# Performance work log

Measured on AMD Instinct MI355X. Metric: run time of the kernel, lower is better.

The kernel has to match this reference:

```python
import jax, jax.numpy as jnp
import numpy as np

N_HEADS = 16
HEAD_DIM = 128
EPS = 1e-6


def _rmsnorm(t, w):
    # RMSNorm over last dim (head_dim)
    var = jnp.mean(jnp.square(t), axis=-1, keepdims=True)
    return t * jax.lax.rsqrt(var + EPS) * w


def _apply_rope(t, freqs):
    # t: [b, s, h, d]; freqs: [s, 1, d//2, 2, 2]
    b, s, h, d = t.shape
    t2 = t.reshape(b, s, h, 2, d // 2)
    t_ = jnp.moveaxis(t2, -2, -1)[..., None, :].astype(jnp.float32)  # [b,s,h,d/2,1,2]
    out = freqs[..., 0] * t_[..., 0] + freqs[..., 1] * t_[..., 1]    # [b,s,h,d/2,2]
    out = jnp.moveaxis(out, -1, -2).reshape(b, s, h, d)
    return out.astype(t.dtype)


def setup_inputs() -> dict:
    key = jax.random.key(0)
    ks = jax.random.split(key, 8)
    B, S, D = 2, 2048, 2048
    inner = N_HEADS * HEAD_DIM
    sc = 1.0 / np.sqrt(D)
    return {
        "x": jax.random.normal(ks[0], (B, S, D), jnp.float32),
        "rope_emb": jax.random.normal(ks[1], (S, 1, HEAD_DIM // 2, 2, 2), jnp.float32),
        "Wq": jax.random.normal(ks[2], (inner, D), jnp.float32) * sc,
        "Wk": jax.random.normal(ks[3], (inner, D), jnp.float32) * sc,
        "Wv": jax.random.normal(ks[4], (inner, D), jnp.float32) * sc,
        "Wo": jax.random.normal(ks[5], (D, inner), jnp.float32) * sc,
        "q_norm_w": jnp.ones((HEAD_DIM,), jnp.float32),
        "k_norm_w": jnp.ones((HEAD_DIM,), jnp.float32),
    }


def reference(x, rope_emb, Wq, Wk, Wv, Wo, q_norm_w, k_norm_w):
    b, s, _ = x.shape
    h, d = N_HEADS, HEAD_DIM
    q = (x @ Wq.T).reshape(b, s, h, d)
    k = (x @ Wk.T).reshape(b, s, h, d)
    v = (x @ Wv.T).reshape(b, s, h, d)
    q = _apply_rope(_rmsnorm(q, q_norm_w), rope_emb)
    k = _apply_rope(_rmsnorm(k, k_norm_w), rope_emb)
    # SDPA, heads-first layout
    qh = jnp.transpose(q, (0, 2, 1, 3))  # [b,h,s,d]
    kh = jnp.transpose(k, (0, 2, 1, 3))
    vh = jnp.transpose(v, (0, 2, 1, 3))
    scale = 1.0 / np.sqrt(d)
    scores = jnp.einsum('bhqd,bhkd->bhqk', qh, kh) * scale
    attn = jax.nn.softmax(scores, axis=-1)
    out = jnp.einsum('bhqk,bhkd->bhqd', attn, vh)  # [b,h,s,d]
    out = jnp.transpose(out, (0, 2, 1, 3)).reshape(b, s, h * d)
    return out @ Wo.T
```

## Files before the change

kernel.cpp:

```cpp
#include <hip/hip_runtime.h>
#include <hip/hip_bf16.h>
#include <stdint.h>

typedef __bf16 bf16;
typedef __bf16 bf16x4 __attribute__((ext_vector_type(4)));
typedef __bf16 bf16x8 __attribute__((ext_vector_type(8)));
typedef float f32x4 __attribute__((ext_vector_type(4)));
typedef float f32x16 __attribute__((ext_vector_type(16)));

#define N_HEADS 16
#define HEAD_DIM 128
#define SEQ 2048
#define DIM 2048
#define BATCH 2
#define MROWS (BATCH * SEQ)
#define NQKV (3 * DIM)
#define SM_SCALE 0.08838834764831845f
#define QSCALE_L2E 0.12751743343563824f
#define SMAX_L2E 34.624680981335122f

#define MFMA16(a, b, c) __builtin_amdgcn_mfma_f32_16x16x32_bf16(a, b, c, 0, 0, 0)

__device__ __forceinline__ bf16 f2b(float f) {
  union { __hip_bfloat16 h; bf16 b; } u;
  u.h = __float2bfloat16(f);
  return u.b;
}

__device__ __forceinline__ uint32_t pack2(float a, float b) {
  union { __hip_bfloat16 h; unsigned short s; } ua, ub;
  ua.h = __float2bfloat16(a); ub.h = __float2bfloat16(b);
  return (uint32_t)ua.s | ((uint32_t)ub.s << 16);
}

__device__ __forceinline__ void async16(const bf16* g, bf16* l) {
  __builtin_amdgcn_global_load_lds(
      (__attribute__((address_space(1))) void*)(uintptr_t)g,
      (__attribute__((address_space(3))) void*)(uintptr_t)l,
      16, 0, 0);
}

__global__ __launch_bounds__(256) void cvt_kernel(const float* __restrict__ src,
                                                  bf16* __restrict__ dst, int n) {
  int i = (blockIdx.x * 256 + threadIdx.x) * 8;
  if (i >= n) return;
  float4 a = *(const float4*)(src + i);
  float4 b = *(const float4*)(src + i + 4);
  bf16x8 o;
  o[0] = f2b(a.x); o[1] = f2b(a.y); o[2] = f2b(a.z); o[3] = f2b(a.w);
  o[4] = f2b(b.x); o[5] = f2b(b.y); o[6] = f2b(b.z); o[7] = f2b(b.w);
  *(bf16x8*)(dst + i) = o;
}

__global__ __launch_bounds__(256) void cvt_w4(const float* __restrict__ w0,
                                              const float* __restrict__ w1,
                                              const float* __restrict__ w2,
                                              const float* __restrict__ w3,
                                              bf16* __restrict__ wqkv,
                                              bf16* __restrict__ wo) {
  const int per = (DIM * DIM) / 8 / 256;
  int which = blockIdx.x / per;
  int i = (blockIdx.x % per) * 256 * 8 + threadIdx.x * 8;
  const float* src = which == 0 ? w0 : which == 1 ? w1 : which == 2 ? w2 : w3;
  bf16* dst = which < 3 ? wqkv + (size_t)which * DIM * DIM : wo;
  float4 a = *(const float4*)(src + i);
  float4 b = *(const float4*)(src + i + 4);
  bf16x8 o;
  o[0] = f2b(a.x); o[1] = f2b(a.y); o[2] = f2b(a.z); o[3] = f2b(a.w);
  o[4] = f2b(b.x); o[5] = f2b(b.y); o[6] = f2b(b.z); o[7] = f2b(b.w);
  *(bf16x8*)(dst + i) = o;
}


#define GBAR() asm volatile("s_barrier" ::: "memory")
#define GWAITL() do { asm volatile("s_waitcnt lgkmcnt(0)" ::: "memory"); \
                      __builtin_amdgcn_sched_barrier(0); } while (0)

__device__ __forceinline__ void g256_stage_half(const bf16* gbase, bf16* lbase,
                                                int w, int lane, int t, int hf) {
  const int kt = t * 64;
#pragma unroll
  for (int i = 0; i < 2; i++) {
    const int rbase = hf * 128 + w * 16 + i * 8;
    const int r = rbase + (lane >> 3);
    async16(gbase + (size_t)r * 2048 + kt + 8 * ((lane & 7) ^ (r & 7)),
            lbase + rbase * 64);
  }
}

__device__ __forceinline__ void g256_lda(const bf16* lbase, int wm, int lm,
                                         int quad, int mh, bf16x8 a[4][2]) {
#pragma unroll
  for (int f = 0; f < 4; f++) {
    const int row = wm * 128 + mh * 64 + f * 16 + lm;
    const char* p = (const char*)lbase + row * 128;
    const int sw = (row & 7) << 4;
#pragma unroll
    for (int s = 0; s < 2; s++)
      a[f][s] = *(const bf16x8*)(p + ((s * 64 + quad * 16) ^ sw));
  }
}

__device__ __forceinline__ void g256_ldb(const bf16* lbase, int wn, int lm,
                                         int quad, int nh, bf16x8 bb[2][2]) {
#pragma unroll
  for (int g = 0; g < 2; g++) {
    const int row = wn * 64 + nh * 32 + g * 16 + lm;
    const char* p = (const char*)lbase + row * 128;
    const int sw = (row & 7) << 4;
#pragma unroll
    for (int s = 0; s < 2; s++)
      bb[g][s] = *(const bf16x8*)(p + ((s * 64 + quad * 16) ^ sw));
  }
}

__device__ __forceinline__ void g256_mma(f32x4 acc[8][4], bf16x8 a[4][2],
                                         bf16x8 bb[2][2], int mh, int nh) {
  __builtin_amdgcn_s_setprio(1);
#pragma unroll
  for (int s = 0; s < 2; s++)
#pragma unroll
    for (int f = 0; f < 4; f++)
#pragma unroll
      for (int g = 0; g < 2; g++)
        acc[mh * 4 + f][nh * 2 + g] =
            MFMA16(a[f][s], bb[g][s], acc[mh * 4 + f][nh * 2 + g]);
  __builtin_amdgcn_s_setprio(0);
}

__device__ __forceinline__ void gemm256_mainloop(
    const bf16* __restrict__ Ag, const bf16* __restrict__ Bg,
    bf16* sA0, bf16* sA1, bf16* sB0, bf16* sB1, f32x4 acc[8][4],
    int w, int lane, int wm, int wn, int lm, int quad) {
  g256_stage_half(Ag, sA0, w, lane, 0, 0);
  g256_stage_half(Ag, sA0, w, lane, 0, 1);
  g256_stage_half(Bg, sB0, w, lane, 0, 0);
  g256_stage_half(Bg, sB0, w, lane, 0, 1);
  g256_stage_half(Ag, sA1, w, lane, 1, 0);
  g256_stage_half(Ag, sA1, w, lane, 1, 1);
  asm volatile("s_waitcnt vmcnt(0)" ::: "memory");
  GBAR();

  bf16x8 a0[4][2], a1[4][2], bb[2][2];

  for (int i = 0; i < 16; i++) {
    const int t1 = 2 * i + 1;
    const int t2 = t1 + 1 < 32 ? t1 + 1 : 31;
    const int t3 = t1 + 2 < 32 ? t1 + 2 : 31;
    g256_lda(sA0, wm, lm, quad, 0, a0);
    g256_ldb(sB0, wn, lm, quad, 0, bb);
    g256_stage_half(Bg, sB1, w, lane, t1, 0);
    GBAR(); GWAITL();
    g256_mma(acc, a0, bb, 0, 0);
    GBAR();
    g256_lda(sA0, wm, lm, quad, 1, a1);
    g256_stage_half(Bg, sB1, w, lane, t1, 1);
    GBAR(); GWAITL();
    g256_mma(acc, a1, bb, 1, 0);
    GBAR();
    g256_ldb(sB0, wn, lm, quad, 1, bb);
    g256_stage_half(Ag, sA0, w, lane, t2, 0);
    GBAR(); GWAITL();
    g256_mma(acc, a1, bb, 1, 1);
    GBAR();
    g256_stage_half(Ag, sA0, w, lane, t2, 1);
    asm volatile("s_waitcnt vmcnt(4)" ::: "memory");
    GBAR(); GWAITL();
    g256_mma(acc, a0, bb, 0, 1);
    GBAR();
    g256_lda(sA1, wm, lm, quad, 0, a0);
    g256_ldb(sB1, wn, lm, quad, 0, bb);
    g256_stage_half(Bg, sB0, w, lane, t2, 0);
    GBAR(); GWAITL();
    g256_mma(acc, a0, bb, 0, 0);
    GBAR();
    g256_lda(sA1, wm, lm, quad, 1, a1);
    g256_stage_half(Bg, sB0, w, lane, t2, 1);
    GBAR(); GWAITL();
    g256_mma(acc, a1, bb, 1, 0);
    GBAR();
    g256_ldb(sB1, wn, lm, quad, 1, bb);
    g256_stage_half(Ag, sA1, w, lane, t3, 0);
    GBAR(); GWAITL();
    g256_mma(acc, a1, bb, 1, 1);
    GBAR();
    g256_stage_half(Ag, sA1, w, lane, t3, 1);
    asm volatile("s_waitcnt vmcnt(4)" ::: "memory");
    GBAR(); GWAITL();
    g256_mma(acc, a0, bb, 0, 1);
    GBAR();
  }
  asm volatile("s_waitcnt vmcnt(0)" ::: "memory");
}

__global__ __launch_bounds__(512, 2) void gemm_qkv(const bf16* __restrict__ X,
                                                   const bf16* __restrict__ W,
                                                   bf16* __restrict__ Q,
                                                   bf16* __restrict__ Kv,
                                                   bf16* __restrict__ VT) {
  __shared__ __align__(16) bf16 sA[2][256 * 64];
  __shared__ __align__(16) bf16 sB[2][256 * 64];
  const int t = threadIdx.x, w = t >> 6, lane = t & 63;
  const int lm = lane & 15, quad = lane >> 4;
  const int wm = w >> 2, wn = w & 3;
  const int bid = blockIdx.x;
  const int swz = (bid & 7) * 48 + (bid >> 3);
  const int bm = swz / 24, bn = swz % 24;
  const int rowBase = bm * 256, colBase = bn * 256;

  f32x4 acc[8][4];
  f32x4 z = {0.f, 0.f, 0.f, 0.f};
#pragma unroll
  for (int i = 0; i < 8; i++)
#pragma unroll
    for (int j = 0; j < 4; j++) acc[i][j] = z;

  gemm256_mainloop(X + (size_t)rowBase * 2048, W + (size_t)colBase * 2048,
                   sA[0], sA[1], sB[0], sB[1], acc, w, lane, wm, wn, lm, quad);

  const int which = colBase >> 11;
  if (which < 2) {
    bf16* dst = which ? Kv : Q;
#pragma unroll
    for (int fi = 0; fi < 8; fi++)
#pragma unroll
      for (int gj = 0; gj < 4; gj++) {
        const int mb = rowBase + wm * 128 + fi * 16 + quad * 4;
        const int nc = (colBase + wn * 64 + gj * 16 + lm) & 2047;
        const int hh = nc >> 7, d = nc & 127;
#pragma unroll
        for (int r = 0; r < 4; r++) {
          const int m = mb + r;
          const int b = m >> 11, s = m & 2047;
          dst[(((size_t)(b * N_HEADS + hh) * SEQ) + s) * HEAD_DIM + d] =
              f2b(acc[fi][gj][r]);
        }
      }
  } else {
#pragma unroll
    for (int fi = 0; fi < 8; fi++)
#pragma unroll
      for (int gj = 0; gj < 4; gj++) {
        const int mb = rowBase + wm * 128 + fi * 16 + quad * 4;
        const int nc = (colBase + wn * 64 + gj * 16 + lm) & 2047;
        const int hh = nc >> 7, d = nc & 127;
        const int b = mb >> 11, s = mb & 2047;
        bf16x4 pk;
#pragma unroll
        for (int r = 0; r < 4; r++) pk[r] = f2b(acc[fi][gj][r]);
        *(bf16x4*)&VT[((size_t)(b * N_HEADS + hh) * HEAD_DIM + d) * SEQ + s] = pk;
      }
  }
}

__device__ __forceinline__ void gemm_tile_mainloop(
    const bf16* __restrict__ A, const bf16* __restrict__ Bw, int K,
    int rowBase, int colBase, bf16* lA, bf16* lB, f32x4 acc[4][4]) {
  const int t = threadIdx.x;
  const int w = t >> 6, lane = t & 63;
  const int lm = lane & 15, quad = lane >> 4;
  const int wr = (w >> 1) * 64, wc = (w & 1) * 64;

  for (int kt = 0; kt < K; kt += 32) {
#pragma unroll
    for (int i = 0; i < 2; i++) {
      const int c = i * 256 + t;
      const int r = c >> 2, cc = (c & 3) << 3;
      async16(A + (size_t)(rowBase + r) * K + (kt + cc), lA + (i * 256 + w * 64) * 8);
      async16(Bw + (size_t)(colBase + r) * K + (kt + cc), lB + (i * 256 + w * 64) * 8);
    }
    asm volatile("s_waitcnt vmcnt(0)" ::: "memory");
    __syncthreads();
    bf16x8 af[4], bfr[4];
#pragma unroll
    for (int f = 0; f < 4; f++)
      af[f] = *(const bf16x8*)(lA + (wr + f * 16 + lm) * 32 + quad * 8);
#pragma unroll
    for (int f = 0; f < 4; f++)
      bfr[f] = *(const bf16x8*)(lB + (wc + f * 16 + lm) * 32 + quad * 8);
#pragma unroll
    for (int fr = 0; fr < 4; fr++)
#pragma unroll
      for (int fc = 0; fc < 4; fc++)
        acc[fr][fc] = MFMA16(af[fr], bfr[fc], acc[fr][fc]);
    __syncthreads();
  }
}

__global__ __launch_bounds__(256) void gemm_out(const bf16* __restrict__ A,
                                                const bf16* __restrict__ W,
                                                float* __restrict__ out) {
  __shared__ __align__(16) bf16 lA[128 * 32];
  __shared__ __align__(16) bf16 lB[128 * 32];
  f32x4 acc[4][4];
  f32x4 z = {0.f, 0.f, 0.f, 0.f};
#pragma unroll
  for (int i = 0; i < 4; i++)
#pragma unroll
    for (int j = 0; j < 4; j++) acc[i][j] = z;

  const int rowBase = blockIdx.y * 128, colBase = blockIdx.x * 128;
  gemm_tile_mainloop(A, W, DIM, rowBase, colBase, lA, lB, acc);

  const int t = threadIdx.x, w = t >> 6, lane = t & 63;
  const int lm = lane & 15, quad = lane >> 4;
  const int wr = (w >> 1) * 64, wc = (w & 1) * 64;
#pragma unroll
  for (int fr = 0; fr < 4; fr++)
#pragma unroll
    for (int fc = 0; fc < 4; fc++)
#pragma unroll
      for (int r = 0; r < 4; r++) {
        int m = rowBase + wr + fr * 16 + quad * 4 + r;
        int n = colBase + wc + fc * 16 + lm;
        out[(size_t)m * DIM + n] = acc[fr][fc][r];
      }
}

__global__ __launch_bounds__(256) void norm_rope(bf16* __restrict__ Q,
                                                 bf16* __restrict__ K,
                                                 const float* __restrict__ rope,
                                                 const float* __restrict__ qw,
                                                 const float* __restrict__ kw) {
  const int t = threadIdx.x, w = t >> 6, lane = t & 63;
  const int rid = blockIdx.x * 4 + w;
  const int which = rid >> 16;
  const int row = rid & 65535;
  bf16* ptr = (which ? K : Q) + (size_t)row * HEAD_DIM;
  const float* nw = which ? kw : qw;
  const int s = row & (SEQ - 1);

  float x0 = (float)ptr[lane];
  float x1 = (float)ptr[lane + 64];
  float ss = x0 * x0 + x1 * x1;
#pragma unroll
  for (int off = 32; off; off >>= 1) ss += __shfl_xor(ss, off);
  float r = rsqrtf(ss * (1.f / 128.f) + 1e-6f);
  float x0n = x0 * r * nw[lane];
  float x1n = x1 * r * nw[lane + 64];
  float4 f = ((const float4*)rope)[s * 64 + lane];
  float y0 = f.x * x0n + f.y * x1n;
  float y1 = f.z * x0n + f.w * x1n;
  if (!which) { y0 *= QSCALE_L2E; y1 *= QSCALE_L2E; }
  ptr[lane] = f2b(y0);
  ptr[lane + 64] = f2b(y1);
}

__global__ __launch_bounds__(256, 2) void attn_kernel(const bf16* __restrict__ Q,
                                                      const bf16* __restrict__ K,
                                                      const bf16* __restrict__ VT,
                                                      bf16* __restrict__ O) {
  __shared__ __align__(16) bf16 Ks[128 * 128];
  __shared__ __align__(16) bf16 Vs[128 * 128];

  const int t = threadIdx.x, w = t >> 6, lane = t & 63;
  const int lq = lane & 31, h = lane >> 5;
  const int bh = blockIdx.x, qt = blockIdx.y;

  bf16x8 qf[8];
  {
    const bf16* Qp = Q + ((size_t)bh * SEQ + qt * 128 + w * 32 + lq) * HEAD_DIM;
#pragma unroll
    for (int ks = 0; ks < 8; ks++)
      qf[ks] = *(const bf16x8*)(Qp + ks * 16 + h * 8);
  }

  f32x16 oacc[4];
#pragma unroll
  for (int nb = 0; nb < 4; nb++)
#pragma unroll
    for (int e = 0; e < 16; e++) oacc[nb][e] = 0.f;
  float rsum = 0.f;

  const bf16* kbase = K + (size_t)bh * SEQ * HEAD_DIM;
  const bf16* vbase = VT + (size_t)bh * HEAD_DIM * SEQ;

  const int srow = w * 32 + (lane >> 4), scc = lane & 15;
  bf16x8 kreg[8], vreg[8];

  auto load_tile = [&](int j) {
    const bf16* kp = kbase + (size_t)j * 128 * HEAD_DIM;
    const bf16* vp = vbase + j * 128;
#pragma unroll
    for (int i = 0; i < 8; i++)
      kreg[i] = *(const bf16x8*)(kp + (size_t)(srow + i * 4) * HEAD_DIM + scc * 8);
#pragma unroll
    for (int i = 0; i < 8; i++)
      vreg[i] = *(const bf16x8*)(vp + (size_t)(srow + i * 4) * SEQ + scc * 8);
  };

  load_tile(0);

  for (int j = 0; j < SEQ / 128; j++) {
#pragma unroll
    for (int i = 0; i < 8; i++) {
      int r = srow + i * 4;
      *(bf16x8*)&Ks[r * 128 + ((scc ^ (r & 15)) << 3)] = kreg[i];
    }
#pragma unroll
    for (int i = 0; i < 8; i++) {
      int d = srow + i * 4;
      *(bf16x8*)&Vs[d * 128 + ((scc ^ (d & 15)) << 3)] = vreg[i];
    }
    __syncthreads();

    if (j + 1 < SEQ / 128) load_tile(j + 1);

#pragma unroll
    for (int bp = 0; bp < 2; bp++) {
      f32x16 sacc[2];
#pragma unroll
      for (int bb = 0; bb < 2; bb++)
#pragma unroll
        for (int e = 0; e < 16; e++) sacc[bb][e] = -SMAX_L2E;
      const int r0 = bp * 64 + lq, r1 = r0 + 32;
#pragma unroll
      for (int ks = 0; ks < 8; ks++) {
        int c = ks * 2 + h;
        bf16x8 kf0 = *(const bf16x8*)&Ks[r0 * 128 + ((c ^ (r0 & 15)) << 3)];
        bf16x8 kf1 = *(const bf16x8*)&Ks[r1 * 128 + ((c ^ (r1 & 15)) << 3)];
        sacc[0] = __builtin_amdgcn_mfma_f32_32x32x16_bf16(kf0, qf[ks], sacc[0], 0, 0, 0);
        sacc[1] = __builtin_amdgcn_mfma_f32_32x32x16_bf16(kf1, qf[ks], sacc[1], 0, 0, 0);
      }

      uint32_t a1[2][4], a2[2][4];
#pragma unroll
      for (int bb = 0; bb < 2; bb++) {
        float e[16];
        float p0 = 0.f, p1 = 0.f, p2 = 0.f, p3 = 0.f;
#pragma unroll
        for (int r = 0; r < 16; r += 4) {
          e[r]     = __builtin_amdgcn_exp2f(sacc[bb][r]);
          e[r + 1] = __builtin_amdgcn_exp2f(sacc[bb][r + 1]);
          e[r + 2] = __builtin_amdgcn_exp2f(sacc[bb][r + 2]);
          e[r + 3] = __builtin_amdgcn_exp2f(sacc[bb][r + 3]);
          p0 += e[r]; p1 += e[r + 1]; p2 += e[r + 2]; p3 += e[r + 3];
        }
        rsum += (p0 + p1) + (p2 + p3);
        uint32_t pk[8];
#pragma unroll
        for (int i = 0; i < 8; i++) pk[i] = pack2(e[2 * i], e[2 * i + 1]);
        uint32_t ta = h ? pk[0] : pk[2], tb = h ? pk[1] : pk[3];
        uint32_t tc = h ? pk[4] : pk[6], td = h ? pk[5] : pk[7];
        uint32_t ra = __shfl_xor((int)ta, 32), rb = __shfl_xor((int)tb, 32);
        uint32_t rc = __shfl_xor((int)tc, 32), rd = __shfl_xor((int)td, 32);
        a1[bb][0] = h ? ra : pk[0]; a1[bb][1] = h ? rb : pk[1];
        a1[bb][2] = h ? pk[2] : ra; a1[bb][3] = h ? pk[3] : rb;
        a2[bb][0] = h ? rc : pk[4]; a2[bb][1] = h ? rd : pk[5];
        a2[bb][2] = h ? pk[6] : rc; a2[bb][3] = h ? pk[7] : rd;
      }

#pragma unroll
      for (int bb = 0; bb < 2; bb++)
#pragma unroll
        for (int ks2 = 0; ks2 < 2; ks2++) {
          union { uint32_t u[4]; bf16x8 v; } ap;
#pragma unroll
          for (int i = 0; i < 4; i++) ap.u[i] = ks2 ? a2[bb][i] : a1[bb][i];
          int c2 = (bp * 2 + bb) * 4 + ks2 * 2 + h;
#pragma unroll
          for (int nb = 0; nb < 4; nb++) {
            int rv = nb * 32 + lq;
            bf16x8 bv = *(const bf16x8*)&Vs[rv * 128 + ((c2 ^ (rv & 15)) << 3)];
            oacc[nb] = __builtin_amdgcn_mfma_f32_32x32x16_bf16(ap.v, bv, oacc[nb], 0, 0, 0);
          }
        }
    }
    __syncthreads();
  }

  rsum += __shfl_xor(rsum, 32);
  float inv = 1.f / rsum;
  const int b = bh >> 4, hh = bh & 15;
#pragma unroll
  for (int nb = 0; nb < 4; nb++)
#pragma unroll
    for (int r = 0; r < 16; r++) {
      int q = (r & 3) + 8 * (r >> 2) + 4 * h;
      float iv = __shfl(inv, q);
      int qg = qt * 128 + w * 32 + q;
      O[((size_t)b * SEQ + qg) * DIM + hh * HEAD_DIM + nb * 32 + lq] = f2b(oacc[nb][r] * iv);
    }
}

extern "C" void kernel_launch(void* const* d_in, const int* in_sizes, int n_in,
                              void* d_out, int out_size, void* d_ws, size_t ws_size,
                              hipStream_t stream) {
  const float* x    = (const float*)d_in[0];
  const float* rope = (const float*)d_in[1];
  const float* Wq   = (const float*)d_in[2];
  const float* Wk   = (const float*)d_in[3];
  const float* Wv   = (const float*)d_in[4];
  const float* Wo   = (const float*)d_in[5];
  const float* qw   = (const float*)d_in[6];
  const float* kw   = (const float*)d_in[7];
  float* out = (float*)d_out;

  char* ws = (char*)d_ws;
  bf16* xb   = (bf16*)ws;
  bf16* wqkv = (bf16*)(ws + (16u << 20));
  bf16* wo   = (bf16*)(ws + (40u << 20));
  bf16* qb   = (bf16*)(ws + (48u << 20));
  bf16* kb   = (bf16*)(ws + (64u << 20));
  bf16* vt   = (bf16*)(ws + (80u << 20));
  bf16* attn = xb;

  const int NX = MROWS * DIM;
  const int NW = DIM * DIM;

  cvt_kernel<<<NX / 8 / 256, 256, 0, stream>>>(x, xb, NX);
  cvt_w4<<<4 * (NW / 8 / 256), 256, 0, stream>>>(Wq, Wk, Wv, Wo, wqkv, wo);

  gemm_qkv<<<(MROWS / 256) * (NQKV / 256), 512, 0, stream>>>(xb, wqkv, qb, kb, vt);
  norm_rope<<<(2 * BATCH * N_HEADS * SEQ) / 4, 256, 0, stream>>>(qb, kb, rope, qw, kw);
  attn_kernel<<<dim3(BATCH * N_HEADS, SEQ / 128), 256, 0, stream>>>(qb, kb, vt, attn);
  gemm_out<<<dim3(DIM / 128, MROWS / 128), 256, 0, stream>>>(attn, wo, out);
}
```

Measured before the change: 416.3 us.

## Shrink QKV GEMM tile to 256x128 with new XCD-aware block mapping

The QKV projection GEMM now uses 256x128 output tiles instead of 256x256, which doubles the block count to 768 and halves the B shared-memory buffers and per-warp accumulators. The warp layout becomes 4x2 with 64x64 per-warp tiles, and the pipelined mainloop is rewritten with four MFMA phases per iteration instead of eight. The block-to-tile mapping is reworked so each XCD gets a contiguous 8x12 region of tiles, aiming for L2 reuse. The aim is better occupancy and load balance across CUs from lower LDS and register use, at the cost of lower arithmetic intensity per tile and more total global traffic.

```diff
diff --git a/kernel.cpp b/kernel.cpp
--- a/kernel.cpp
+++ b/kernel.cpp
@@ -76,23 +76,31 @@
 #define GWAITL() do { asm volatile("s_waitcnt lgkmcnt(0)" ::: "memory"); \
                       __builtin_amdgcn_sched_barrier(0); } while (0)
 
-__device__ __forceinline__ void g256_stage_half(const bf16* gbase, bf16* lbase,
-                                                int w, int lane, int t, int hf) {
-  const int kt = t * 64;
+__device__ __forceinline__ void g_stage128(const bf16* gbase, bf16* lbase,
+                                           int w, int lane, int t, int rowoff) {
 #pragma unroll
   for (int i = 0; i < 2; i++) {
-    const int rbase = hf * 128 + w * 16 + i * 8;
+    const int rbase = rowoff + w * 16 + i * 8;
     const int r = rbase + (lane >> 3);
-    async16(gbase + (size_t)r * 2048 + kt + 8 * ((lane & 7) ^ (r & 7)),
+    async16(gbase + (size_t)r * 2048 + t * 64 + 8 * ((lane & 7) ^ (r & 7)),
             lbase + rbase * 64);
   }
 }
-
-__device__ __forceinline__ void g256_lda(const bf16* lbase, int wm, int lm,
-                                         int quad, int mh, bf16x8 a[4][2]) {
+__device__ __forceinline__ void g_stageA(const bf16* Ag, bf16* sA,
+                                         int w, int lane, int t) {
+  g_stage128(Ag, sA, w, lane, t, 0);
+  g_stage128(Ag, sA, w, lane, t, 128);
+}
+__device__ __forceinline__ void g_stageB(const bf16* Bg, bf16* sB,
+                                         int w, int lane, int t) {
+  g_stage128(Bg, sB, w, lane, t, 0);
+}
+
+__device__ __forceinline__ void g_lda(const bf16* lbase, int wm, int lm,
+                                      int quad, bf16x8 a[4][2]) {
 #pragma unroll
   for (int f = 0; f < 4; f++) {
-    const int row = wm * 128 + mh * 64 + f * 16 + lm;
+    const int row = wm * 64 + f * 16 + lm;
     const char* p = (const char*)lbase + row * 128;
     const int sw = (row & 7) << 4;
 #pragma unroll
@@ -101,8 +109,8 @@
   }
 }
 
-__device__ __forceinline__ void g256_ldb(const bf16* lbase, int wn, int lm,
-                                         int quad, int nh, bf16x8 bb[2][2]) {
+__device__ __forceinline__ void g_ldb(const bf16* lbase, int wn, int nh, int lm,
+                                      int quad, bf16x8 bb[2][2]) {
 #pragma unroll
   for (int g = 0; g < 2; g++) {
     const int row = wn * 64 + nh * 32 + g * 16 + lm;
@@ -114,8 +122,8 @@
   }
 }
 
-__device__ __forceinline__ void g256_mma(f32x4 acc[8][4], bf16x8 a[4][2],
-                                         bf16x8 bb[2][2], int mh, int nh) {
+__device__ __forceinline__ void g_mma(f32x4 acc[4][4], bf16x8 a[4][2],
+                                      bf16x8 bb[2][2], int nh) {
   __builtin_amdgcn_s_setprio(1);
 #pragma unroll
   for (int s = 0; s < 2; s++)
@@ -123,74 +131,8 @@
     for (int f = 0; f < 4; f++)
 #pragma unroll
       for (int g = 0; g < 2; g++)
-        acc[mh * 4 + f][nh * 2 + g] =
-            MFMA16(a[f][s], bb[g][s], acc[mh * 4 + f][nh * 2 + g]);
+        acc[f][nh * 2 + g] = MFMA16(a[f][s], bb[g][s], acc[f][nh * 2 + g]);
   __builtin_amdgcn_s_setprio(0);
-}
-
-__device__ __forceinline__ void gemm256_mainloop(
-    const bf16* __restrict__ Ag, const bf16* __restrict__ Bg,
-    bf16* sA0, bf16* sA1, bf16* sB0, bf16* sB1, f32x4 acc[8][4],
-    int w, int lane, int wm, int wn, int lm, int quad) {
-  g256_stage_half(Ag, sA0, w, lane, 0, 0);
-  g256_stage_half(Ag, sA0, w, lane, 0, 1);
-  g256_stage_half(Bg, sB0, w, lane, 0, 0);
-  g256_stage_half(Bg, sB0, w, lane, 0, 1);
-  g256_stage_half(Ag, sA1, w, lane, 1, 0);
-  g256_stage_half(Ag, sA1, w, lane, 1, 1);
-  asm volatile("s_waitcnt vmcnt(0)" ::: "memory");
-  GBAR();
-
-  bf16x8 a0[4][2], a1[4][2], bb[2][2];
-
-  for (int i = 0; i < 16; i++) {
-    const int t1 = 2 * i + 1;
-    const int t2 = t1 + 1 < 32 ? t1 + 1 : 31;
-    const int t3 = t1 + 2 < 32 ? t1 + 2 : 31;
-    g256_lda(sA0, wm, lm, quad, 0, a0);
-    g256_ldb(sB0, wn, lm, quad, 0, bb);
-    g256_stage_half(Bg, sB1, w, lane, t1, 0);
-    GBAR(); GWAITL();
-    g256_mma(acc, a0, bb, 0, 0);
-    GBAR();
-    g256_lda(sA0, wm, lm, quad, 1, a1);
-    g256_stage_half(Bg, sB1, w, lane, t1, 1);
-    GBAR(); GWAITL();
-    g256_mma(acc, a1, bb, 1, 0);
-    GBAR();
-    g256_ldb(sB0, wn, lm, quad, 1, bb);
-    g256_stage_half(Ag, sA0, w, lane, t2, 0);
-    GBAR(); GWAITL();
-    g256_mma(acc, a1, bb, 1, 1);
-    GBAR();
-    g256_stage_half(Ag, sA0, w, lane, t2, 1);
-    asm volatile("s_waitcnt vmcnt(4)" ::: "memory");
-    GBAR(); GWAITL();
-    g256_mma(acc, a0, bb, 0, 1);
-    GBAR();
-    g256_lda(sA1, wm, lm, quad, 0, a0);
-    g256_ldb(sB1, wn, lm, quad, 0, bb);
-    g256_stage_half(Bg, sB0, w, lane, t2, 0);
-    GBAR(); GWAITL();
-    g256_mma(acc, a0, bb, 0, 0);
-    GBAR();
-    g256_lda(sA1, wm, lm, quad, 1, a1);
-    g256_stage_half(Bg, sB0, w, lane, t2, 1);
-    GBAR(); GWAITL();
-    g256_mma(acc, a1, bb, 1, 0);
-    GBAR();
-    g256_ldb(sB1, wn, lm, quad, 1, bb);
-    g256_stage_half(Ag, sA1, w, lane, t3, 0);
-    GBAR(); GWAITL();
-    g256_mma(acc, a1, bb, 1, 1);
-    GBAR();
-    g256_stage_half(Ag, sA1, w, lane, t3, 1);
-    asm volatile("s_waitcnt vmcnt(4)" ::: "memory");
-    GBAR(); GWAITL();
-    g256_mma(acc, a0, bb, 0, 1);
-    GBAR();
-  }
-  asm volatile("s_waitcnt vmcnt(0)" ::: "memory");
 }
 
 __global__ __launch_bounds__(512, 2) void gemm_qkv(const bf16* __restrict__ X,
@@ -199,33 +141,73 @@
                                                    bf16* __restrict__ Kv,
                                                    bf16* __restrict__ VT) {
   __shared__ __align__(16) bf16 sA[2][256 * 64];
-  __shared__ __align__(16) bf16 sB[2][256 * 64];
+  __shared__ __align__(16) bf16 sB[2][128 * 64];
   const int t = threadIdx.x, w = t >> 6, lane = t & 63;
   const int lm = lane & 15, quad = lane >> 4;
-  const int wm = w >> 2, wn = w & 3;
+  const int wm = w >> 1, wn = w & 1;
   const int bid = blockIdx.x;
-  const int swz = (bid & 7) * 48 + (bid >> 3);
-  const int bm = swz / 24, bn = swz % 24;
-  const int rowBase = bm * 256, colBase = bn * 256;
-
-  f32x4 acc[8][4];
+  const int xcd = bid & 7, loc = bid >> 3;
+  const int bm = (xcd >> 2) * 8 + loc / 12;
+  const int bn = (xcd & 3) * 12 + loc % 12;
+  const int rowBase = bm * 256, colBase = bn * 128;
+
+  f32x4 acc[4][4];
   f32x4 z = {0.f, 0.f, 0.f, 0.f};
 #pragma unroll
-  for (int i = 0; i < 8; i++)
+  for (int i = 0; i < 4; i++)
 #pragma unroll
     for (int j = 0; j < 4; j++) acc[i][j] = z;
 
-  gemm256_mainloop(X + (size_t)rowBase * 2048, W + (size_t)colBase * 2048,
-                   sA[0], sA[1], sB[0], sB[1], acc, w, lane, wm, wn, lm, quad);
+  const bf16* Ag = X + (size_t)rowBase * 2048;
+  const bf16* Bg = W + (size_t)colBase * 2048;
+
+  g_stageA(Ag, sA[0], w, lane, 0);
+  g_stageB(Bg, sB[0], w, lane, 0);
+  g_stageA(Ag, sA[1], w, lane, 1);
+  asm volatile("s_waitcnt vmcnt(0)" ::: "memory");
+  GBAR();
+
+  bf16x8 a[4][2], bb[2][2];
+
+  for (int i = 0; i < 16; i++) {
+    const int t1 = 2 * i + 1;
+    const int t2 = t1 + 1 < 32 ? t1 + 1 : 31;
+    const int t3 = t1 + 2 < 32 ? t1 + 2 : 31;
+    g_lda(sA[0], wm, lm, quad, a);
+    g_ldb(sB[0], wn, 0, lm, quad, bb);
+    g_stageB(Bg, sB[1], w, lane, t1);
+    GBAR(); GWAITL();
+    g_mma(acc, a, bb, 0);
+    GBAR();
+    g_ldb(sB[0], wn, 1, lm, quad, bb);
+    g_stageA(Ag, sA[0], w, lane, t2);
+    asm volatile("s_waitcnt vmcnt(4)" ::: "memory");
+    GBAR(); GWAITL();
+    g_mma(acc, a, bb, 1);
+    GBAR();
+    g_lda(sA[1], wm, lm, quad, a);
+    g_ldb(sB[1], wn, 0, lm, quad, bb);
+    g_stageB(Bg, sB[0], w, lane, t2);
+    GBAR(); GWAITL();
+    g_mma(acc, a, bb, 0);
+    GBAR();
+    g_ldb(sB[1], wn, 1, lm, quad, bb);
+    g_stageA(Ag, sA[1], w, lane, t3);
+    asm volatile("s_waitcnt vmcnt(4)" ::: "memory");
+    GBAR(); GWAITL();
+    g_mma(acc, a, bb, 1);
+    GBAR();
+  }
+  asm volatile("s_waitcnt vmcnt(0)" ::: "memory");
 
   const int which = colBase >> 11;
   if (which < 2) {
     bf16* dst = which ? Kv : Q;
 #pragma unroll
-    for (int fi = 0; fi < 8; fi++)
+    for (int fi = 0; fi < 4; fi++)
 #pragma unroll
       for (int gj = 0; gj < 4; gj++) {
-        const int mb = rowBase + wm * 128 + fi * 16 + quad * 4;
+        const int mb = rowBase + wm * 64 + fi * 16 + quad * 4;
         const int nc = (colBase + wn * 64 + gj * 16 + lm) & 2047;
         const int hh = nc >> 7, d = nc & 127;
 #pragma unroll
@@ -238,10 +220,10 @@
       }
   } else {
 #pragma unroll
-    for (int fi = 0; fi < 8; fi++)
+    for (int fi = 0; fi < 4; fi++)
 #pragma unroll
       for (int gj = 0; gj < 4; gj++) {
-        const int mb = rowBase + wm * 128 + fi * 16 + quad * 4;
+        const int mb = rowBase + wm * 64 + fi * 16 + quad * 4;
         const int nc = (colBase + wn * 64 + gj * 16 + lm) & 2047;
         const int hh = nc >> 7, d = nc & 127;
         const int b = mb >> 11, s = mb & 2047;
@@ -511,7 +493,7 @@
   cvt_kernel<<<NX / 8 / 256, 256, 0, stream>>>(x, xb, NX);
   cvt_w4<<<4 * (NW / 8 / 256), 256, 0, stream>>>(Wq, Wk, Wv, Wo, wqkv, wo);
 
-  gemm_qkv<<<(MROWS / 256) * (NQKV / 256), 512, 0, stream>>>(xb, wqkv, qb, kb, vt);
+  gemm_qkv<<<(MROWS / 256) * (NQKV / 128), 512, 0, stream>>>(xb, wqkv, qb, kb, vt);
   norm_rope<<<(2 * BATCH * N_HEADS * SEQ) / 4, 256, 0, stream>>>(qb, kb, rope, qw, kw);
   attn_kernel<<<dim3(BATCH * N_HEADS, SEQ / 128), 256, 0, stream>>>(qb, kb, vt, attn);
   gemm_out<<<dim3(DIM / 128, MROWS / 128), 256, 0, stream>>>(attn, wo, out);
```

Result: no change. 415.5 us (-0.2%).
